# Performance work log

Hardware: AMD Instinct MI355X
Metric: run time of the kernel (lower is better)

Reference implementation:

```python
import jax, jax.numpy as jnp
import numpy as np

N = 50000
E = 1600000
IN_C = 128
HID = 64
HEADS = 4
OUT_C = 64
NEG_SLOPE = 0.2


def gat_layer(x, src, dst, W, a_src, a_dst, b, heads, ch):
    # x: [N, F_in], W: [F_in, heads*ch], a_src/a_dst: [heads, ch], b: [heads*ch]
    n = x.shape[0]
    h = (x @ W).reshape(n, heads, ch)                       # [N, H, C]
    alpha_s = jnp.einsum('nhc,hc->nh', h, a_src)            # [N, H]
    alpha_d = jnp.einsum('nhc,hc->nh', h, a_dst)
    e = jax.nn.leaky_relu(alpha_s[src] + alpha_d[dst], NEG_SLOPE)  # [Et, H]
    # segment softmax over incoming edges of each dst node (self-loops guarantee non-empty)
    m = jax.ops.segment_max(e, dst, num_segments=n)
    ex = jnp.exp(e - m[dst])
    denom = jax.ops.segment_sum(ex, dst, num_segments=n)
    alpha = ex / (denom[dst] + 1e-16)                       # [Et, H]
    out = jax.ops.segment_sum(h[src] * alpha[:, :, None], dst, num_segments=n)  # [N,H,C]
    return out.reshape(n, heads * ch) + b


def setup_inputs() -> dict:
    key = jax.random.key(0)
    ks = jax.random.split(key, 10)
    x = jax.random.normal(ks[0], (N, IN_C), dtype=jnp.float32)
    edge_index = jax.random.randint(ks[1], (2, E), 0, N, dtype=jnp.int64)
    s = 0.1
    W1 = jax.random.normal(ks[2], (IN_C, HEADS * HID), dtype=jnp.float32) * s
    a_src1 = jax.random.normal(ks[3], (HEADS, HID), dtype=jnp.float32) * s
    a_dst1 = jax.random.normal(ks[4], (HEADS, HID), dtype=jnp.float32) * s
    b1 = jnp.zeros((HEADS * HID,), dtype=jnp.float32)
    W2 = jax.random.normal(ks[5], (HEADS * HID, OUT_C), dtype=jnp.float32) * s
    a_src2 = jax.random.normal(ks[6], (1, OUT_C), dtype=jnp.float32) * s
    a_dst2 = jax.random.normal(ks[7], (1, OUT_C), dtype=jnp.float32) * s
    b2 = jnp.zeros((OUT_C,), dtype=jnp.float32)
    return {"x": x, "edge_index": edge_index, "W1": W1, "a_src1": a_src1,
            "a_dst1": a_dst1, "b1": b1, "W2": W2, "a_src2": a_src2,
            "a_dst2": a_dst2, "b2": b2}


def reference(x, edge_index, W1, a_src1, a_dst1, b1, W2, a_src2, a_dst2, b2):
    # add self-loops (PyG GATConv default)
    loops = jnp.arange(N, dtype=edge_index.dtype)
    src = jnp.concatenate([edge_index[0], loops])
    dst = jnp.concatenate([edge_index[1], loops])
    h = gat_layer(x, src, dst, W1, a_src1, a_dst1, b1, HEADS, HID)
    h = jax.nn.relu(h)
    out = gat_layer(h, src, dst, W2, a_src2, a_dst2, b2, 1, OUT_C)
    return out
```

## Files before the change

### kernel.cpp

```cpp
#include <hip/hip_runtime.h>
#include <cstdint>
#include <cstddef>

#define IN_C 128

typedef _Float16 __attribute__((ext_vector_type(4))) half4v;
typedef _Float16 __attribute__((ext_vector_type(8))) f16x8;
typedef float    __attribute__((ext_vector_type(4))) f32x4;

static __device__ __forceinline__ float lrelu(float x) { return x > 0.f ? x : 0.2f * x; }

static __device__ __forceinline__ float h16_to_f(unsigned short u) {
  union { unsigned short u; _Float16 h; } c; c.u = u;
  return (float)c.h;
}
static __device__ __forceinline__ unsigned pack2h(float a, float b) {
  union { _Float16 h[2]; unsigned u; } c;
  c.h[0] = (_Float16)a; c.h[1] = (_Float16)b;
  return c.u;
}

__global__ void k_zero_i32(int* __restrict__ p, int n) {
  int i = blockIdx.x * 256 + threadIdx.x;
  if (i < n) p[i] = 0;
}

__global__ void k_count(const int* __restrict__ ei_dst, int* __restrict__ cnt, int E, int Et) {
  int e = blockIdx.x * 256 + threadIdx.x;
  if (e >= Et) return;
  int d = (e < E) ? ei_dst[e] : (e - E);
  atomicAdd(&cnt[d], 1);
}

__global__ void k_scan1(const int* __restrict__ cnt, int* __restrict__ loc,
                        int* __restrict__ bsum, int n) {
  int tid = threadIdx.x;
  int i = blockIdx.x * 256 + tid;
  int v = (i < n) ? cnt[i] : 0;
  int lane = tid & 63, w = tid >> 6;
  int s = v;
#pragma unroll
  for (int off = 1; off < 64; off <<= 1) {
    int t = __shfl_up(s, off);
    if (lane >= off) s += t;
  }
  __shared__ int wt[4];
  if (lane == 63) wt[w] = s;
  __syncthreads();
  int add = 0;
#pragma unroll
  for (int k = 0; k < 4; ++k)
    if (k < w) add += wt[k];
  int incl = s + add;
  if (i < n) loc[i] = incl - v;
  if (tid == 255) bsum[blockIdx.x] = incl;
}

__global__ void k_scan3b(const int* __restrict__ loc, const int* __restrict__ bsum,
                         int* __restrict__ row_ptr, int* __restrict__ fill, int n, int nb) {
  int tid = threadIdx.x, b = blockIdx.x;
  int lane = tid & 63, w = tid >> 6;
  int p = 0, t = 0;
  for (int k = tid; k < nb; k += 256) {
    int v = bsum[k];
    t += v;
    if (k < b) p += v;
  }
#pragma unroll
  for (int off = 1; off < 64; off <<= 1) {
    p += __shfl_xor(p, off);
    t += __shfl_xor(t, off);
  }
  __shared__ int sp_[4], st_[4];
  if (lane == 0) { sp_[w] = p; st_[w] = t; }
  __syncthreads();
  p = sp_[0] + sp_[1] + sp_[2] + sp_[3];
  t = st_[0] + st_[1] + st_[2] + st_[3];
  int i = b * 256 + tid;
  if (i < n) {
    int v = loc[i] + p;
    row_ptr[i] = v;
    fill[i] = v;
  }
  if (b == 0 && tid == 0) row_ptr[n] = t;
}

__global__ void k_scatter_fused(const int* __restrict__ ei_src, const int* __restrict__ ei_dst,
                                int* __restrict__ fill,
                                const float* __restrict__ as1, const float* __restrict__ ad1,
                                uint4* __restrict__ recs, int E, int Et, int nPerReg, int n) {
  int r = blockIdx.x & 7;
  int e = (blockIdx.x >> 3) * 256 + threadIdx.x;
  if (e >= Et) return;
  int d = (e < E) ? ei_dst[e] : (e - E);
  int lo = r * nPerReg;
  int hi = (r == 7) ? n : lo + nPerReg;
  if (d < lo || d >= hi) return;
  int s = (e < E) ? ei_src[e] : d;
  int pos = atomicAdd(&fill[d], 1);
  float4 a = *(const float4*)&as1[s * 4];
  float4 b = *(const float4*)&ad1[d * 4];
  unsigned w01 = pack2h(__expf(lrelu(a.x + b.x)), __expf(lrelu(a.y + b.y)));
  unsigned w23 = pack2h(__expf(lrelu(a.z + b.z)), __expf(lrelu(a.w + b.w)));
  recs[pos] = make_uint4((unsigned)s, (unsigned)d, w01, w23);
}

__global__ void k_xh(const float* __restrict__ x, _Float16* __restrict__ xh, int n4) {
  int i = blockIdx.x * 256 + threadIdx.x;
  if (i >= n4) return;
  float4 v = *(const float4*)&x[i * 4];
  half4v o;
  o.x = (_Float16)v.x; o.y = (_Float16)v.y; o.z = (_Float16)v.z; o.w = (_Float16)v.w;
  *(half4v*)&xh[i * 4] = o;
}

__global__ void k_wts(const float* __restrict__ W1, const float* __restrict__ W2,
                      _Float16* __restrict__ W1t, _Float16* __restrict__ W2t) {
  int i = blockIdx.x * 256 + threadIdx.x;
  if (i < 128 * 256) {
    int k = i / 256, nn = i % 256;
    W1t[(size_t)nn * 128 + k] = (_Float16)W1[i];
  } else {
    int j = i - 128 * 256;
    if (j < 256 * 64) {
      int k = j / 64, nn = j % 64;
      W2t[(size_t)nn * 256 + k] = (_Float16)W2[j];
    }
  }
}

__launch_bounds__(256)
__global__ void k_gemm1_a(const _Float16* __restrict__ A, const _Float16* __restrict__ Bt,
                          const float* __restrict__ a_s, const float* __restrict__ a_d,
                          _Float16* __restrict__ C, float* __restrict__ as1,
                          float* __restrict__ ad1, int M) {
  int w = threadIdx.x >> 6, lane = threadIdx.x & 63;
  int r = lane & 15, kg = lane >> 4;
  int m0 = blockIdx.x * 64 + w * 16;
  f32x4 acc[16];
#pragma unroll
  for (int c = 0; c < 16; ++c) acc[c] = (f32x4){0.f, 0.f, 0.f, 0.f};
  int mA = m0 + r; if (mA > M - 1) mA = M - 1;
  const _Float16* Arow = A + (size_t)mA * 128 + kg * 8;
#pragma unroll
  for (int k0 = 0; k0 < 128; k0 += 32) {
    f16x8 a = *(const f16x8*)(Arow + k0);
#pragma unroll
    for (int c = 0; c < 16; ++c) {
      f16x8 b = *(const f16x8*)&Bt[(size_t)(c * 16 + r) * 128 + k0 + kg * 8];
      acc[c] = __builtin_amdgcn_mfma_f32_16x16x32_f16(a, b, acc[c], 0, 0, 0);
    }
  }
  float sp[4][4] = {}, dp[4][4] = {};
#pragma unroll
  for (int c = 0; c < 16; ++c) {
    float asv = a_s[c * 16 + r];
    float adv = a_d[c * 16 + r];
#pragma unroll
    for (int j = 0; j < 4; ++j) {
      float v = acc[c][j];
      sp[c >> 2][j] += v * asv;
      dp[c >> 2][j] += v * adv;
    }
  }
#pragma unroll
  for (int off = 1; off < 16; off <<= 1) {
#pragma unroll
    for (int h = 0; h < 4; ++h)
#pragma unroll
      for (int j = 0; j < 4; ++j) {
        sp[h][j] += __shfl_xor(sp[h][j], off);
        dp[h][j] += __shfl_xor(dp[h][j], off);
      }
  }
#pragma unroll
  for (int c = 0; c < 16; ++c) {
#pragma unroll
    for (int j = 0; j < 4; ++j) {
      int m = m0 + kg * 4 + j;
      if (m < M) C[(size_t)m * 256 + c * 16 + r] = (_Float16)acc[c][j];
    }
  }
  if (r == 0) {
#pragma unroll
    for (int j = 0; j < 4; ++j) {
      int m = m0 + kg * 4 + j;
      if (m < M) {
#pragma unroll
        for (int h = 0; h < 4; ++h) {
          as1[m * 4 + h] = sp[h][j];
          ad1[m * 4 + h] = dp[h][j];
        }
      }
    }
  }
}

__launch_bounds__(256)
__global__ void k_gemm2_a(const _Float16* __restrict__ A, const _Float16* __restrict__ Bt,
                          const float* __restrict__ a_s, const float* __restrict__ a_d,
                          _Float16* __restrict__ C, float* __restrict__ as2,
                          float* __restrict__ ad2, int M) {
  int w = threadIdx.x >> 6, lane = threadIdx.x & 63;
  int r = lane & 15, kg = lane >> 4;
  int m0 = blockIdx.x * 64 + w * 16;
  f32x4 acc[4];
#pragma unroll
  for (int c = 0; c < 4; ++c) acc[c] = (f32x4){0.f, 0.f, 0.f, 0.f};
  int mA = m0 + r; if (mA > M - 1) mA = M - 1;
  const _Float16* Arow = A + (size_t)mA * 256 + kg * 8;
#pragma unroll
  for (int k0 = 0; k0 < 256; k0 += 32) {
    f16x8 a = *(const f16x8*)(Arow + k0);
#pragma unroll
    for (int c = 0; c < 4; ++c) {
      f16x8 b = *(const f16x8*)&Bt[(size_t)(c * 16 + r) * 256 + k0 + kg * 8];
      acc[c] = __builtin_amdgcn_mfma_f32_16x16x32_f16(a, b, acc[c], 0, 0, 0);
    }
  }
  float sp[4] = {}, dp[4] = {};
#pragma unroll
  for (int c = 0; c < 4; ++c) {
    float asv = a_s[c * 16 + r];
    float adv = a_d[c * 16 + r];
#pragma unroll
    for (int j = 0; j < 4; ++j) {
      float v = acc[c][j];
      sp[j] += v * asv;
      dp[j] += v * adv;
    }
  }
#pragma unroll
  for (int off = 1; off < 16; off <<= 1) {
#pragma unroll
    for (int j = 0; j < 4; ++j) {
      sp[j] += __shfl_xor(sp[j], off);
      dp[j] += __shfl_xor(dp[j], off);
    }
  }
#pragma unroll
  for (int c = 0; c < 4; ++c) {
#pragma unroll
    for (int j = 0; j < 4; ++j) {
      int m = m0 + kg * 4 + j;
      if (m < M) C[(size_t)m * 64 + c * 16 + r] = (_Float16)acc[c][j];
    }
  }
  if (r == 0) {
#pragma unroll
    for (int j = 0; j < 4; ++j) {
      int m = m0 + kg * 4 + j;
      if (m < M) { as2[m] = sp[j]; ad2[m] = dp[j]; }
    }
  }
}

__launch_bounds__(256)
__global__ void k_aggr1(const int* __restrict__ row_ptr, const uint4* __restrict__ recs,
                        const _Float16* __restrict__ h1h, const float* __restrict__ b1,
                        _Float16* __restrict__ hrelu_h, int n) {
  int wave = threadIdx.x >> 6, lane = threadIdx.x & 63;
  int node = blockIdx.x * 4 + wave;
  if (node >= n) return;
  int beg = row_ptr[node], end = row_ptr[node + 1];
  int g = lane >> 4, l16 = lane & 15;
  int ch0 = l16 * 16;
  int myh = l16 >> 2;
  float acc[16] = {};
  float dsum = 0.f;
  for (int i = beg; i < end; i += 8) {
    int iA = i + g, iB = i + 4 + g;
    int sA = 0, sB = 0;
    float wA = 0.f, wB = 0.f;
    if (iA < end) {
      uint4 rc = recs[iA];
      sA = (int)rc.x;
      unsigned wp = (myh & 2) ? rc.w : rc.z;
      wA = h16_to_f((myh & 1) ? (unsigned short)(wp >> 16) : (unsigned short)(wp & 0xffffu));
    }
    if (iB < end) {
      uint4 rc = recs[iB];
      sB = (int)rc.x;
      unsigned wp = (myh & 2) ? rc.w : rc.z;
      wB = h16_to_f((myh & 1) ? (unsigned short)(wp >> 16) : (unsigned short)(wp & 0xffffu));
    }
    const _Float16* pA = &h1h[(size_t)sA * 256 + ch0];
    const _Float16* pB = &h1h[(size_t)sB * 256 + ch0];
    f16x8 a0 = *(const f16x8*)pA;
    f16x8 a1 = *(const f16x8*)(pA + 8);
    f16x8 c0 = *(const f16x8*)pB;
    f16x8 c1 = *(const f16x8*)(pB + 8);
    dsum += wA + wB;
#pragma unroll
    for (int j = 0; j < 8; ++j) acc[j] += wA * (float)a0[j];
#pragma unroll
    for (int j = 0; j < 8; ++j) acc[8 + j] += wA * (float)a1[j];
#pragma unroll
    for (int j = 0; j < 8; ++j) acc[j] += wB * (float)c0[j];
#pragma unroll
    for (int j = 0; j < 8; ++j) acc[8 + j] += wB * (float)c1[j];
  }
#pragma unroll
  for (int off = 16; off < 64; off <<= 1) {
    dsum += __shfl_xor(dsum, off);
#pragma unroll
    for (int j = 0; j < 16; ++j) acc[j] += __shfl_xor(acc[j], off);
  }
  if (g == 0) {
    float inv = 1.0f / (dsum + 1e-16f);
    f16x8 oA, oB;
#pragma unroll
    for (int j = 0; j < 8; ++j) {
      oA[j] = (_Float16)fmaxf(acc[j] * inv + b1[ch0 + j], 0.f);
      oB[j] = (_Float16)fmaxf(acc[8 + j] * inv + b1[ch0 + 8 + j], 0.f);
    }
    _Float16* op = &hrelu_h[(size_t)node * 256 + ch0];
    *(f16x8*)op = oA;
    *(f16x8*)(op + 8) = oB;
  }
}

__launch_bounds__(256)
__global__ void k_aggr2(const int* __restrict__ row_ptr, const uint4* __restrict__ recs,
                        const float* __restrict__ as2, const float* __restrict__ ad2,
                        const _Float16* __restrict__ h2h, const float* __restrict__ b2,
                        float* __restrict__ out, int n) {
  int wave = threadIdx.x >> 6, lane = threadIdx.x & 63;
  int node = blockIdx.x * 4 + wave;
  if (node >= n) return;
  int beg = row_ptr[node], end = row_ptr[node + 1];
  float adm = ad2[node];
  int g = lane >> 4, l16 = lane & 15;
  int ch0 = l16 * 4;
  float acc[4] = {};
  float dsum = 0.f;
  for (int i = beg; i < end; i += 8) {
    int iA = i + g, iB = i + 4 + g;
    int sA = 0, sB = 0;
    float wA = 0.f, wB = 0.f;
    if (iA < end) {
      sA = (int)recs[iA].x;
      wA = __expf(lrelu(as2[sA] + adm));
    }
    if (iB < end) {
      sB = (int)recs[iB].x;
      wB = __expf(lrelu(as2[sB] + adm));
    }
    half4v hA = *(const half4v*)&h2h[(size_t)sA * 64 + ch0];
    half4v hB = *(const half4v*)&h2h[(size_t)sB * 64 + ch0];
    dsum += wA + wB;
    acc[0] += wA * (float)hA.x + wB * (float)hB.x;
    acc[1] += wA * (float)hA.y + wB * (float)hB.y;
    acc[2] += wA * (float)hA.z + wB * (float)hB.z;
    acc[3] += wA * (float)hA.w + wB * (float)hB.w;
  }
#pragma unroll
  for (int off = 16; off < 64; off <<= 1) {
    dsum += __shfl_xor(dsum, off);
#pragma unroll
    for (int j = 0; j < 4; ++j) acc[j] += __shfl_xor(acc[j], off);
  }
  if (g == 0) {
    float inv = 1.0f / (dsum + 1e-16f);
    float4 o;
    o.x = acc[0] * inv + b2[ch0];
    o.y = acc[1] * inv + b2[ch0 + 1];
    o.z = acc[2] * inv + b2[ch0 + 2];
    o.w = acc[3] * inv + b2[ch0 + 3];
    *(float4*)&out[(size_t)node * 64 + ch0] = o;
  }
}

extern "C" void kernel_launch(void* const* d_in, const int* in_sizes, int n_in,
                              void* d_out, int out_size, void* d_ws, size_t ws_size,
                              hipStream_t stream) {
  const float* x    = (const float*)d_in[0];
  const int*   ei   = (const int*)d_in[1];
  const float* W1   = (const float*)d_in[2];
  const float* a_s1 = (const float*)d_in[3];
  const float* a_d1 = (const float*)d_in[4];
  const float* b1   = (const float*)d_in[5];
  const float* W2   = (const float*)d_in[6];
  const float* a_s2 = (const float*)d_in[7];
  const float* a_d2 = (const float*)d_in[8];
  const float* b2   = (const float*)d_in[9];
  float* out = (float*)d_out;

  const int n  = in_sizes[0] / IN_C;
  const int E  = in_sizes[1] / 2;
  const int Et = E + n;
  const int* ei_src = ei;
  const int* ei_dst = ei + E;

  char* ws = (char*)d_ws;
  size_t off = 0;
  auto alloc = [&](size_t bytes) -> void* {
    void* p = ws + off;
    off = (off + bytes + 255) & ~(size_t)255;
    return p;
  };
  _Float16* xh      = (_Float16*)alloc((size_t)n * 128 * 2);
  _Float16* W1t     = (_Float16*)alloc((size_t)256 * 128 * 2);
  _Float16* W2t     = (_Float16*)alloc((size_t)64 * 256 * 2);
  _Float16* h1h     = (_Float16*)alloc((size_t)n * 256 * 2);
  _Float16* hrelu_h = (_Float16*)alloc((size_t)n * 256 * 2);
  _Float16* h2h     = (_Float16*)alloc((size_t)n * 64 * 2);
  float* as1        = (float*)alloc((size_t)n * 4 * 4);
  float* ad1        = (float*)alloc((size_t)n * 4 * 4);
  float* as2        = (float*)alloc((size_t)n * 4);
  float* ad2        = (float*)alloc((size_t)n * 4);
  int* cnt          = (int*)alloc((size_t)n * 4);
  int* loc          = (int*)alloc((size_t)n * 4);
  int* row_ptr      = (int*)alloc((size_t)(n + 1) * 4);
  int* fill         = (int*)alloc((size_t)n * 4);
  int* bsum         = (int*)alloc((size_t)256 * 4);
  uint4* recs       = (uint4*)alloc((size_t)Et * 16);

  int eb  = (Et + 255) / 256;
  int nb  = (n + 255) / 256;
  int nw  = (n + 3) / 4;
  int gx1 = (n + 63) / 64;
  int nPerReg = (n + 7) / 8;

  hipLaunchKernelGGL(k_zero_i32, dim3(nb), dim3(256), 0, stream, cnt, n);
  hipLaunchKernelGGL(k_count, dim3(eb), dim3(256), 0, stream, ei_dst, cnt, E, Et);
  hipLaunchKernelGGL(k_scan1, dim3(nb), dim3(256), 0, stream, cnt, loc, bsum, n);
  hipLaunchKernelGGL(k_scan3b, dim3(nb), dim3(256), 0, stream, loc, bsum, row_ptr, fill, n, nb);

  hipLaunchKernelGGL(k_xh, dim3((n * 128 / 4 + 255) / 256), dim3(256), 0, stream, x, xh, n * 128 / 4);
  hipLaunchKernelGGL(k_wts, dim3((128 * 256 + 256 * 64 + 255) / 256), dim3(256), 0, stream,
                     W1, W2, W1t, W2t);

  hipLaunchKernelGGL(k_gemm1_a, dim3(gx1), dim3(256), 0, stream,
                     xh, W1t, a_s1, a_d1, h1h, as1, ad1, n);
  hipLaunchKernelGGL(k_scatter_fused, dim3(eb * 8), dim3(256), 0, stream,
                     ei_src, ei_dst, fill, as1, ad1, recs, E, Et, nPerReg, n);
  hipLaunchKernelGGL(k_aggr1, dim3(nw), dim3(256), 0, stream, row_ptr, recs, h1h, b1, hrelu_h, n);

  hipLaunchKernelGGL(k_gemm2_a, dim3(gx1), dim3(256), 0, stream,
                     hrelu_h, W2t, a_s2, a_d2, h2h, as2, ad2, n);
  hipLaunchKernelGGL(k_aggr2, dim3(nw), dim3(256), 0, stream,
                     row_ptr, recs, as2, ad2, h2h, b2, out, n);
}
```

Measured before the change: 402.3 us.

## Add nontemporal loads/stores, region-partition count, fuse prep kernels, compact srcs for aggr2

Several unrelated changes land together. Edge counting is partitioned into 8 destination regions, like the scatter, so atomics stay local. Input and weight conversion are merged into one prep kernel, and a memset replaces the zero kernel, cutting launches. Many loads and stores become nontemporal to avoid cache pollution. Scatter also writes a compact 32-bit source array, so aggr2 reads 4 bytes per edge instead of 16-byte records. The aggregation loops drop the two-edge unroll to one edge per group per step, which may reduce memory-level parallelism.

```diff
diff --git a/kernel.cpp b/kernel.cpp
--- a/kernel.cpp
+++ b/kernel.cpp
@@ -7,6 +7,7 @@
 typedef _Float16 __attribute__((ext_vector_type(4))) half4v;
 typedef _Float16 __attribute__((ext_vector_type(8))) f16x8;
 typedef float    __attribute__((ext_vector_type(4))) f32x4;
+typedef unsigned __attribute__((ext_vector_type(4))) u32x4;
 
 static __device__ __forceinline__ float lrelu(float x) { return x > 0.f ? x : 0.2f * x; }
 
@@ -20,15 +21,15 @@
   return c.u;
 }
 
-__global__ void k_zero_i32(int* __restrict__ p, int n) {
-  int i = blockIdx.x * 256 + threadIdx.x;
-  if (i < n) p[i] = 0;
-}
-
-__global__ void k_count(const int* __restrict__ ei_dst, int* __restrict__ cnt, int E, int Et) {
-  int e = blockIdx.x * 256 + threadIdx.x;
+__global__ void k_count(const int* __restrict__ ei_dst, int* __restrict__ cnt,
+                        int E, int Et, int nPerReg, int n) {
+  int r = blockIdx.x & 7;
+  int e = (blockIdx.x >> 3) * 256 + threadIdx.x;
   if (e >= Et) return;
-  int d = (e < E) ? ei_dst[e] : (e - E);
+  int d = (e < E) ? __builtin_nontemporal_load(&ei_dst[e]) : (e - E);
+  int lo = r * nPerReg;
+  int hi = (r == 7) ? n : lo + nPerReg;
+  if (d < lo || d >= hi) return;
   atomicAdd(&cnt[d], 1);
 }
 
@@ -88,43 +89,49 @@
 __global__ void k_scatter_fused(const int* __restrict__ ei_src, const int* __restrict__ ei_dst,
                                 int* __restrict__ fill,
                                 const float* __restrict__ as1, const float* __restrict__ ad1,
-                                uint4* __restrict__ recs, int E, int Et, int nPerReg, int n) {
+                                u32x4* __restrict__ recs, int* __restrict__ srcs32,
+                                int E, int Et, int nPerReg, int n) {
   int r = blockIdx.x & 7;
   int e = (blockIdx.x >> 3) * 256 + threadIdx.x;
   if (e >= Et) return;
-  int d = (e < E) ? ei_dst[e] : (e - E);
+  int d = (e < E) ? __builtin_nontemporal_load(&ei_dst[e]) : (e - E);
   int lo = r * nPerReg;
   int hi = (r == 7) ? n : lo + nPerReg;
   if (d < lo || d >= hi) return;
-  int s = (e < E) ? ei_src[e] : d;
+  int s = (e < E) ? __builtin_nontemporal_load(&ei_src[e]) : d;
   int pos = atomicAdd(&fill[d], 1);
   float4 a = *(const float4*)&as1[s * 4];
   float4 b = *(const float4*)&ad1[d * 4];
   unsigned w01 = pack2h(__expf(lrelu(a.x + b.x)), __expf(lrelu(a.y + b.y)));
   unsigned w23 = pack2h(__expf(lrelu(a.z + b.z)), __expf(lrelu(a.w + b.w)));
-  recs[pos] = make_uint4((unsigned)s, (unsigned)d, w01, w23);
-}
-
-__global__ void k_xh(const float* __restrict__ x, _Float16* __restrict__ xh, int n4) {
-  int i = blockIdx.x * 256 + threadIdx.x;
-  if (i >= n4) return;
-  float4 v = *(const float4*)&x[i * 4];
-  half4v o;
-  o.x = (_Float16)v.x; o.y = (_Float16)v.y; o.z = (_Float16)v.z; o.w = (_Float16)v.w;
-  *(half4v*)&xh[i * 4] = o;
-}
-
-__global__ void k_wts(const float* __restrict__ W1, const float* __restrict__ W2,
-                      _Float16* __restrict__ W1t, _Float16* __restrict__ W2t) {
-  int i = blockIdx.x * 256 + threadIdx.x;
-  if (i < 128 * 256) {
-    int k = i / 256, nn = i % 256;
-    W1t[(size_t)nn * 128 + k] = (_Float16)W1[i];
+  u32x4 rec = {(unsigned)s, (unsigned)d, w01, w23};
+  __builtin_nontemporal_store(rec, &recs[pos]);
+  __builtin_nontemporal_store(s, &srcs32[pos]);
+}
+
+__global__ void k_prep(const float* __restrict__ x, const float* __restrict__ W1,
+                       const float* __restrict__ W2, _Float16* __restrict__ xh,
+                       _Float16* __restrict__ W1t, _Float16* __restrict__ W2t,
+                       int n4, int xb) {
+  int b = blockIdx.x;
+  if (b < xb) {
+    int i = b * 256 + threadIdx.x;
+    if (i >= n4) return;
+    f32x4 v = __builtin_nontemporal_load((const f32x4*)&x[i * 4]);
+    half4v o;
+    o.x = (_Float16)v.x; o.y = (_Float16)v.y; o.z = (_Float16)v.z; o.w = (_Float16)v.w;
+    *(half4v*)&xh[i * 4] = o;
   } else {
-    int j = i - 128 * 256;
-    if (j < 256 * 64) {
-      int k = j / 64, nn = j % 64;
-      W2t[(size_t)nn * 256 + k] = (_Float16)W2[j];
+    int i = (b - xb) * 256 + threadIdx.x;
+    if (i < 128 * 256) {
+      int k = i / 256, nn = i % 256;
+      W1t[(size_t)nn * 128 + k] = (_Float16)W1[i];
+    } else {
+      int j = i - 128 * 256;
+      if (j < 256 * 64) {
+        int k = j / 64, nn = j % 64;
+        W2t[(size_t)nn * 256 + k] = (_Float16)W2[j];
+      }
     }
   }
 }
@@ -144,7 +151,7 @@
   const _Float16* Arow = A + (size_t)mA * 128 + kg * 8;
 #pragma unroll
   for (int k0 = 0; k0 < 128; k0 += 32) {
-    f16x8 a = *(const f16x8*)(Arow + k0);
+    f16x8 a = __builtin_nontemporal_load((const f16x8*)(Arow + k0));
 #pragma unroll
     for (int c = 0; c < 16; ++c) {
       f16x8 b = *(const f16x8*)&Bt[(size_t)(c * 16 + r) * 128 + k0 + kg * 8];
@@ -211,7 +218,7 @@
   const _Float16* Arow = A + (size_t)mA * 256 + kg * 8;
 #pragma unroll
   for (int k0 = 0; k0 < 256; k0 += 32) {
-    f16x8 a = *(const f16x8*)(Arow + k0);
+    f16x8 a = __builtin_nontemporal_load((const f16x8*)(Arow + k0));
 #pragma unroll
     for (int c = 0; c < 4; ++c) {
       f16x8 b = *(const f16x8*)&Bt[(size_t)(c * 16 + r) * 256 + k0 + kg * 8];
@@ -256,7 +263,7 @@
 }
 
 __launch_bounds__(256)
-__global__ void k_aggr1(const int* __restrict__ row_ptr, const uint4* __restrict__ recs,
+__global__ void k_aggr1(const int* __restrict__ row_ptr, const u32x4* __restrict__ recs,
                         const _Float16* __restrict__ h1h, const float* __restrict__ b1,
                         _Float16* __restrict__ hrelu_h, int n) {
   int wave = threadIdx.x >> 6, lane = threadIdx.x & 63;
@@ -268,37 +275,23 @@
   int myh = l16 >> 2;
   float acc[16] = {};
   float dsum = 0.f;
-  for (int i = beg; i < end; i += 8) {
-    int iA = i + g, iB = i + 4 + g;
-    int sA = 0, sB = 0;
-    float wA = 0.f, wB = 0.f;
-    if (iA < end) {
-      uint4 rc = recs[iA];
-      sA = (int)rc.x;
+  for (int i = beg; i < end; i += 4) {
+    int idx = i + g;
+    int s = 0; float w = 0.f;
+    if (idx < end) {
+      u32x4 rc = __builtin_nontemporal_load(&recs[idx]);
+      s = (int)rc.x;
       unsigned wp = (myh & 2) ? rc.w : rc.z;
-      wA = h16_to_f((myh & 1) ? (unsigned short)(wp >> 16) : (unsigned short)(wp & 0xffffu));
-    }
-    if (iB < end) {
-      uint4 rc = recs[iB];
-      sB = (int)rc.x;
-      unsigned wp = (myh & 2) ? rc.w : rc.z;
-      wB = h16_to_f((myh & 1) ? (unsigned short)(wp >> 16) : (unsigned short)(wp & 0xffffu));
-    }
-    const _Float16* pA = &h1h[(size_t)sA * 256 + ch0];
-    const _Float16* pB = &h1h[(size_t)sB * 256 + ch0];
-    f16x8 a0 = *(const f16x8*)pA;
-    f16x8 a1 = *(const f16x8*)(pA + 8);
-    f16x8 c0 = *(const f16x8*)pB;
-    f16x8 c1 = *(const f16x8*)(pB + 8);
-    dsum += wA + wB;
-#pragma unroll
-    for (int j = 0; j < 8; ++j) acc[j] += wA * (float)a0[j];
-#pragma unroll
-    for (int j = 0; j < 8; ++j) acc[8 + j] += wA * (float)a1[j];
-#pragma unroll
-    for (int j = 0; j < 8; ++j) acc[j] += wB * (float)c0[j];
-#pragma unroll
-    for (int j = 0; j < 8; ++j) acc[8 + j] += wB * (float)c1[j];
+      w = h16_to_f((myh & 1) ? (unsigned short)(wp >> 16) : (unsigned short)(wp & 0xffffu));
+    }
+    const _Float16* hp = &h1h[(size_t)s * 256 + ch0];
+    f16x8 hA = *(const f16x8*)hp;
+    f16x8 hB = *(const f16x8*)(hp + 8);
+    dsum += w;
+#pragma unroll
+    for (int j = 0; j < 8; ++j) acc[j] += w * (float)hA[j];
+#pragma unroll
+    for (int j = 0; j < 8; ++j) acc[8 + j] += w * (float)hB[j];
   }
 #pragma unroll
   for (int off = 16; off < 64; off <<= 1) {
@@ -315,13 +308,13 @@
       oB[j] = (_Float16)fmaxf(acc[8 + j] * inv + b1[ch0 + 8 + j], 0.f);
     }
     _Float16* op = &hrelu_h[(size_t)node * 256 + ch0];
-    *(f16x8*)op = oA;
-    *(f16x8*)(op + 8) = oB;
+    __builtin_nontemporal_store(oA, (f16x8*)op);
+    __builtin_nontemporal_store(oB, (f16x8*)(op + 8));
   }
 }
 
 __launch_bounds__(256)
-__global__ void k_aggr2(const int* __restrict__ row_ptr, const uint4* __restrict__ recs,
+__global__ void k_aggr2(const int* __restrict__ row_ptr, const int* __restrict__ srcs32,
                         const float* __restrict__ as2, const float* __restrict__ ad2,
                         const _Float16* __restrict__ h2h, const float* __restrict__ b2,
                         float* __restrict__ out, int n) {
@@ -334,25 +327,17 @@
   int ch0 = l16 * 4;
   float acc[4] = {};
   float dsum = 0.f;
-  for (int i = beg; i < end; i += 8) {
-    int iA = i + g, iB = i + 4 + g;
-    int sA = 0, sB = 0;
-    float wA = 0.f, wB = 0.f;
-    if (iA < end) {
-      sA = (int)recs[iA].x;
-      wA = __expf(lrelu(as2[sA] + adm));
-    }
-    if (iB < end) {
-      sB = (int)recs[iB].x;
-      wB = __expf(lrelu(as2[sB] + adm));
-    }
-    half4v hA = *(const half4v*)&h2h[(size_t)sA * 64 + ch0];
-    half4v hB = *(const half4v*)&h2h[(size_t)sB * 64 + ch0];
-    dsum += wA + wB;
-    acc[0] += wA * (float)hA.x + wB * (float)hB.x;
-    acc[1] += wA * (float)hA.y + wB * (float)hB.y;
-    acc[2] += wA * (float)hA.z + wB * (float)hB.z;
-    acc[3] += wA * (float)hA.w + wB * (float)hB.w;
+  for (int i = beg; i < end; i += 4) {
+    int idx = i + g;
+    int s = 0; float w = 0.f;
+    if (idx < end) {
+      s = __builtin_nontemporal_load(&srcs32[idx]);
+      w = __expf(lrelu(as2[s] + adm));
+    }
+    half4v hv = *(const half4v*)&h2h[(size_t)s * 64 + ch0];
+    dsum += w;
+    acc[0] += w * (float)hv.x; acc[1] += w * (float)hv.y;
+    acc[2] += w * (float)hv.z; acc[3] += w * (float)hv.w;
   }
 #pragma unroll
   for (int off = 16; off < 64; off <<= 1) {
@@ -362,12 +347,12 @@
   }
   if (g == 0) {
     float inv = 1.0f / (dsum + 1e-16f);
-    float4 o;
+    f32x4 o;
     o.x = acc[0] * inv + b2[ch0];
     o.y = acc[1] * inv + b2[ch0 + 1];
     o.z = acc[2] * inv + b2[ch0 + 2];
     o.w = acc[3] * inv + b2[ch0 + 3];
-    *(float4*)&out[(size_t)node * 64 + ch0] = o;
+    __builtin_nontemporal_store(o, (f32x4*)&out[(size_t)node * 64 + ch0]);
   }
 }
 
@@ -414,31 +399,33 @@
   int* row_ptr      = (int*)alloc((size_t)(n + 1) * 4);
   int* fill         = (int*)alloc((size_t)n * 4);
   int* bsum         = (int*)alloc((size_t)256 * 4);
-  uint4* recs       = (uint4*)alloc((size_t)Et * 16);
+  u32x4* recs       = (u32x4*)alloc((size_t)Et * 16);
+  int* srcs32       = (int*)alloc((size_t)Et * 4);
 
   int eb  = (Et + 255) / 256;
   int nb  = (n + 255) / 256;
   int nw  = (n + 3) / 4;
   int gx1 = (n + 63) / 64;
   int nPerReg = (n + 7) / 8;
-
-  hipLaunchKernelGGL(k_zero_i32, dim3(nb), dim3(256), 0, stream, cnt, n);
-  hipLaunchKernelGGL(k_count, dim3(eb), dim3(256), 0, stream, ei_dst, cnt, E, Et);
+  int n4  = n * 128 / 4;
+  int xb  = (n4 + 255) / 256;
+  int wb  = (128 * 256 + 256 * 64 + 255) / 256;
+
+  (void)hipMemsetAsync(cnt, 0, (size_t)n * 4, stream);
+  hipLaunchKernelGGL(k_count, dim3(eb * 8), dim3(256), 0, stream, ei_dst, cnt, E, Et, nPerReg, n);
   hipLaunchKernelGGL(k_scan1, dim3(nb), dim3(256), 0, stream, cnt, loc, bsum, n);
   hipLaunchKernelGGL(k_scan3b, dim3(nb), dim3(256), 0, stream, loc, bsum, row_ptr, fill, n, nb);
 
-  hipLaunchKernelGGL(k_xh, dim3((n * 128 / 4 + 255) / 256), dim3(256), 0, stream, x, xh, n * 128 / 4);
-  hipLaunchKernelGGL(k_wts, dim3((128 * 256 + 256 * 64 + 255) / 256), dim3(256), 0, stream,
-                     W1, W2, W1t, W2t);
+  hipLaunchKernelGGL(k_prep, dim3(xb + wb), dim3(256), 0, stream, x, W1, W2, xh, W1t, W2t, n4, xb);
 
   hipLaunchKernelGGL(k_gemm1_a, dim3(gx1), dim3(256), 0, stream,
                      xh, W1t, a_s1, a_d1, h1h, as1, ad1, n);
   hipLaunchKernelGGL(k_scatter_fused, dim3(eb * 8), dim3(256), 0, stream,
-                     ei_src, ei_dst, fill, as1, ad1, recs, E, Et, nPerReg, n);
+                     ei_src, ei_dst, fill, as1, ad1, recs, srcs32, E, Et, nPerReg, n);
   hipLaunchKernelGGL(k_aggr1, dim3(nw), dim3(256), 0, stream, row_ptr, recs, h1h, b1, hrelu_h, n);
 
   hipLaunchKernelGGL(k_gemm2_a, dim3(gx1), dim3(256), 0, stream,
                      hrelu_h, W2t, a_s2, a_d2, h2h, as2, ad2, n);
   hipLaunchKernelGGL(k_aggr2, dim3(nw), dim3(256), 0, stream,
-                     row_ptr, recs, as2, ad2, h2h, b2, out, n);
-}
+                     row_ptr, srcs32, as2, ad2, h2h, b2, out, n);
+}
```

Result: slower. 494.2 us (+22.8%).
